# Kernel optimization log

Measured on AMD Instinct MI355X. Metric: run time of the kernel, lower is better.

The kernel has to match this reference:

```python
import jax, jax.numpy as jnp
import numpy as np

D = 512
MOMENTUM = 0.99
NEG_INF = -1.0e9


def setup_inputs() -> dict:
    key = jax.random.key(0)
    ks = jax.random.split(key, 16)
    B, Lq, Lk = 16, 1024, 1024
    s = 0.02
    inp = {
        "uncond_q": jax.random.normal(ks[0], (B, D), jnp.float32),
        "q": jax.random.normal(ks[1], (B, Lq, D), jnp.float32),
        "k": jax.random.normal(ks[2], (B, Lk, D), jnp.float32),
        "v": jax.random.normal(ks[3], (B, Lk, D), jnp.float32),
        "src_key_padding_mask": jax.random.randint(ks[4], (B, Lk), 0, 2) > 0,
        "fallback_score": jnp.zeros((1,), jnp.float32),
        # parameters (torch Linear: y = x @ W.T + b)
        "Wv": jax.random.normal(ks[5], (D, D), jnp.float32) * s,
        "bv": jnp.zeros((D,), jnp.float32),
        "Wf": jax.random.normal(ks[6], (D, D), jnp.float32) * s,
        "bf": jnp.zeros((D,), jnp.float32),
        "W1": jax.random.normal(ks[7], (D, D), jnp.float32) * s,
        "b1": jnp.zeros((D,), jnp.float32),
        "W2": jax.random.normal(ks[8], (D // 2, D), jnp.float32) * s,
        "b2": jnp.zeros((D // 2,), jnp.float32),
        "W3": jax.random.normal(ks[9], (1, D // 2), jnp.float32) * s,
        "b3": jnp.zeros((1,), jnp.float32),
    }
    return inp


def _scorer(x, W1, b1, W2, b2, W3, b3):
    h = jax.nn.relu(x @ W1.T + b1)
    h = jax.nn.relu(h @ W2.T + b2)
    return jnp.tanh(h @ W3.T + b3)


def reference(uncond_q, q, k, v, src_key_padding_mask, fallback_score,
              Wv, bv, Wf, bf, W1, b1, W2, b2, W3, b3):
    B, Lq, _ = q.shape
    v_p = v @ Wv.T + bv                                  # [B,Lk,D]
    default_values = (uncond_q @ Wf.T + bf)[:, None, :]  # [B,1,D]

    scores = jnp.einsum('bqd,bkd->bqk', q, k) / jnp.sqrt(jnp.float32(D))

    # EMA fallback-score update (training mode), detached from grads
    bmax = jax.lax.stop_gradient(scores.max())
    bmin = jax.lax.stop_gradient(scores.min())
    fb = MOMENTUM * fallback_score[0] + (1.0 - MOMENTUM) * (bmax + bmin) / 2.0

    scores = jnp.where(src_key_padding_mask[:, None, :], NEG_INF, scores)
    fb_col = jnp.broadcast_to(fb, (B, Lq, 1))
    scores = jnp.concatenate([scores, fb_col], axis=-1)   # [B,Lq,Lk+1]
    weights = jax.nn.softmax(scores, axis=-1)

    v_padded = jnp.concatenate([v_p, default_values], axis=1)  # [B,Lk+1,D]
    out = jnp.einsum('bqk,bkd->bqd', weights, v_padded)

    return (_scorer(out, W1, b1, W2, b2, W3, b3),
            _scorer(default_values, W1, b1, W2, b2, W3, b3))
```

## Files before the change

### kernel.cpp

```cpp
#include <hip/hip_runtime.h>

typedef _Float16 f16;
typedef f16  f16x8 __attribute__((ext_vector_type(8)));
typedef f16  f16x4 __attribute__((ext_vector_type(4)));
typedef float f32x4 __attribute__((ext_vector_type(4)));

__device__ __forceinline__ void gld_lds16(const f16* g, void* l) {
  __builtin_amdgcn_global_load_lds((const __attribute__((address_space(1))) void*)g,
                                   (__attribute__((address_space(3))) void*)l,
                                   16, 0, 0);
}

enum { EPI_SCORES = 0, EPI_RELU = 2, EPI_OUT = 3, EPI_BIASR = 4 };

template<int EPI, bool XMAP>
__global__ __launch_bounds__(256)
void gemm_bt(const f16* __restrict__ A, const f16* __restrict__ B, void* __restrict__ C,
             int lda, int ldb, int ldc, int K,
             long long sA, long long sB, long long sC,
             const float* __restrict__ bias, float scale,
             float* __restrict__ mmarr, int nmm,
             const float* __restrict__ wfb, const float* __restrict__ dvv,
             int nx, int nbz)
{
  __shared__ __align__(16) f16 As[3][128][32];
  __shared__ __align__(16) f16 Bs[3][128][32];
  const int tid  = threadIdx.x;
  const int lane = tid & 63;
  const int w    = tid >> 6;
  const int wm   = w >> 1, wn = w & 1;

  const int lin = blockIdx.x;
  int bz, bj;
  if constexpr (XMAP) {
    const int xcd = lin & 7, rest = lin >> 3;
    const int grp = rest / nbz;
    bj = rest - grp * nbz;
    bz = xcd + (grp << 3);
  } else {
    bz = lin / nbz; bj = lin - bz * nbz;
  }
  const int m0 = (bj / nx) * 128, n0 = (bj % nx) * 128;
  const f16* Ab = A + (size_t)bz * sA + (size_t)m0 * lda;
  const f16* Bb = B + (size_t)bz * sB + (size_t)n0 * ldb;

  f32x4 acc[4][4] = {};
  const int nsteps = K >> 5;

#define STAGE(bufb, ks)                                                              \
  {                                                                                  \
    const int k0_ = (ks) << 5;                                                       \
    _Pragma("unroll")                                                                \
    for (int i = 0; i < 2; ++i) {                                                    \
      const int ci = i * 256 + tid;                                                  \
      const int r  = ci >> 2;                                                        \
      const int sg = (ci & 3) ^ ((r >> 1) & 3);                                      \
      gld_lds16(Ab + (size_t)r * lda + k0_ + sg * 8,                                 \
                (char*)As + (bufb) + (size_t)(i * 256 + w * 64) * 16);               \
      gld_lds16(Bb + (size_t)r * ldb + k0_ + sg * 8,                                 \
                (char*)Bs + (bufb) + (size_t)(i * 256 + w * 64) * 16);               \
    }                                                                                \
  }

  STAGE(0, 0)
  STAGE(8192, 1)

  const int elemoff = (((lane >> 4) ^ ((lane >> 1) & 3)) << 3);

  int cur = 0;
  for (int t = 0; t < nsteps; ++t) {
    if (t + 1 < nsteps) asm volatile("s_waitcnt vmcnt(4)" ::: "memory");
    else                asm volatile("s_waitcnt vmcnt(0)" ::: "memory");
    __builtin_amdgcn_s_barrier();
    __builtin_amdgcn_sched_barrier(0);
    int st = cur + 2; if (st >= 3) st -= 3;
    if (t + 2 < nsteps) STAGE(st * 8192, t + 2)
    f16x8 af[4], bfr[4];
#pragma unroll
    for (int m = 0; m < 4; ++m)
      af[m] = *(const f16x8*)&As[cur][wm * 64 + m * 16 + (lane & 15)][elemoff];
#pragma unroll
    for (int n = 0; n < 4; ++n)
      bfr[n] = *(const f16x8*)&Bs[cur][wn * 64 + n * 16 + (lane & 15)][elemoff];
    __builtin_amdgcn_s_setprio(1);
#pragma unroll
    for (int m = 0; m < 4; ++m)
#pragma unroll
      for (int n = 0; n < 4; ++n)
        acc[m][n] = __builtin_amdgcn_mfma_f32_16x16x32_f16(af[m], bfr[n], acc[m][n], 0, 0, 0);
    __builtin_amdgcn_s_setprio(0);
    cur = (cur + 1 == 3) ? 0 : cur + 1;
  }
#undef STAGE

  const int col_l = lane & 15;
  const int row_l = (lane >> 4) << 2;

  {
    f16* Ch = (f16*)C + (size_t)bz * sC + (size_t)m0 * ldc + n0;
#pragma unroll
    for (int m = 0; m < 4; ++m)
#pragma unroll
      for (int n = 0; n < 4; ++n)
#pragma unroll
        for (int r = 0; r < 4; ++r) {
          const int rr = wm * 64 + m * 16 + row_l + r;
          const int cc = wn * 64 + n * 16 + col_l;
          float val = acc[m][n][r];
          if constexpr (EPI == EPI_RELU) { val += bias[n0 + cc]; val = fmaxf(val, 0.0f); }
          if constexpr (EPI == EPI_BIASR) val += bias[m0 + rr];
          if constexpr (EPI == EPI_OUT)
            val += wfb[bz * 1024 + m0 + rr] * dvv[bz * 512 + n0 + cc];
          Ch[(size_t)rr * ldc + cc] = (f16)val;
        }
  }
  (void)scale; (void)mmarr; (void)nmm;
}

__global__ __launch_bounds__(512, 2)
void gemm256_scores(const f16* __restrict__ A, const f16* __restrict__ B, f16* __restrict__ C,
                    float scale, float* __restrict__ mmarr)
{
  __shared__ __align__(16) f16 As[3][256][32];
  __shared__ __align__(16) f16 Bs[3][256][32];
  __shared__ float redm[8], redn[8];
  const int tid  = threadIdx.x;
  const int lane = tid & 63;
  const int w    = tid >> 6;
  const int wm   = w >> 2, wn = w & 3;
  const int lin  = blockIdx.x;
  const int xcd = lin & 7, rest = lin >> 3;
  const int bj  = rest & 15;
  const int bz  = xcd + ((rest >> 4) << 3);
  const int m0 = (bj >> 2) * 256, n0 = (bj & 3) * 256;
  const f16* Ab = A + (size_t)bz * 524288 + (size_t)m0 * 512;
  const f16* Bb = B + (size_t)bz * 524288 + (size_t)n0 * 512;

  f32x4 acc[8][4] = {};

#define STAGE2(bufb, ks)                                                             \
  {                                                                                  \
    const int k0_ = (ks) << 5;                                                       \
    _Pragma("unroll")                                                                \
    for (int i = 0; i < 2; ++i) {                                                    \
      const int ci = i * 512 + tid;                                                  \
      const int r  = ci >> 2;                                                        \
      const int sg = (ci & 3) ^ ((r >> 1) & 3);                                      \
      gld_lds16(Ab + (size_t)r * 512 + k0_ + sg * 8,                                 \
                (char*)As + (bufb) + (size_t)(i * 512 + w * 64) * 16);               \
      gld_lds16(Bb + (size_t)r * 512 + k0_ + sg * 8,                                 \
                (char*)Bs + (bufb) + (size_t)(i * 512 + w * 64) * 16);               \
    }                                                                                \
  }

  STAGE2(0, 0)
  STAGE2(16384, 1)

  const int elemoff = (((lane >> 4) ^ ((lane >> 1) & 3)) << 3);

  int cur = 0;
  for (int t = 0; t < 16; ++t) {
    if (t + 1 < 16) asm volatile("s_waitcnt vmcnt(4)" ::: "memory");
    else            asm volatile("s_waitcnt vmcnt(0)" ::: "memory");
    __builtin_amdgcn_s_barrier();
    __builtin_amdgcn_sched_barrier(0);
    int st = cur + 2; if (st >= 3) st -= 3;
    if (t + 2 < 16) STAGE2(st * 16384, t + 2)
    f16x8 af[8], bfr[4];
#pragma unroll
    for (int m = 0; m < 8; ++m)
      af[m] = *(const f16x8*)&As[cur][wm * 128 + m * 16 + (lane & 15)][elemoff];
#pragma unroll
    for (int n = 0; n < 4; ++n)
      bfr[n] = *(const f16x8*)&Bs[cur][wn * 64 + n * 16 + (lane & 15)][elemoff];
    __builtin_amdgcn_s_setprio(1);
#pragma unroll
    for (int m = 0; m < 8; ++m)
#pragma unroll
      for (int n = 0; n < 4; ++n)
        acc[m][n] = __builtin_amdgcn_mfma_f32_16x16x32_f16(af[m], bfr[n], acc[m][n], 0, 0, 0);
    __builtin_amdgcn_s_setprio(0);
    cur = (cur + 1 == 3) ? 0 : cur + 1;
  }
#undef STAGE2

  const int col_l = lane & 15;
  const int row_l = (lane >> 4) << 2;
  f16* Ch = C + (size_t)bz * 1048576 + (size_t)m0 * 1024 + n0;
  float lmax = -3.402823466e38f, lmin = 3.402823466e38f;
#pragma unroll
  for (int m = 0; m < 8; ++m)
#pragma unroll
    for (int n = 0; n < 4; ++n)
#pragma unroll
      for (int r = 0; r < 4; ++r) {
        float val = acc[m][n][r] * scale;
        lmax = fmaxf(lmax, val); lmin = fminf(lmin, val);
        Ch[(size_t)(wm * 128 + m * 16 + row_l + r) * 1024 + (wn * 64 + n * 16 + col_l)] = (f16)val;
      }
#pragma unroll
  for (int off = 32; off >= 1; off >>= 1) {
    lmax = fmaxf(lmax, __shfl_xor(lmax, off));
    lmin = fminf(lmin, __shfl_xor(lmin, off));
  }
  if (lane == 0) { redm[w] = lmax; redn[w] = lmin; }
  __syncthreads();
  if (tid == 0) {
    float gm = redm[0], gn = redn[0];
#pragma unroll
    for (int i = 1; i < 8; ++i) { gm = fmaxf(gm, redm[i]); gn = fminf(gn, redn[i]); }
    mmarr[lin] = gm; mmarr[256 + lin] = gn;
  }
}

__global__ __launch_bounds__(256)
void reduce_mm(const float* __restrict__ mmarr, int n,
               const float* __restrict__ fallback, float* __restrict__ fbv,
               const unsigned char* __restrict__ mask, unsigned* __restrict__ mm)
{
  __shared__ float rm[4], rn[4];
  __shared__ int redc[256];
  const int lane = threadIdx.x & 63, w = threadIdx.x >> 6;
  float mx = -3.402823466e38f, mn = 3.402823466e38f;
  for (int i = threadIdx.x; i < n; i += 256) {
    mx = fmaxf(mx, mmarr[i]);
    mn = fminf(mn, mmarr[n + i]);
  }
#pragma unroll
  for (int off = 32; off >= 1; off >>= 1) {
    mx = fmaxf(mx, __shfl_xor(mx, off));
    mn = fminf(mn, __shfl_xor(mn, off));
  }
  if (lane == 0) { rm[w] = mx; rn[w] = mn; }
  int c = 0;
  for (int i = threadIdx.x; i < 16384; i += 256) c += (mask[i] != 0) ? 1 : 0;
  redc[threadIdx.x] = c;
  __syncthreads();
  for (int s = 128; s > 0; s >>= 1) {
    if (threadIdx.x < s) redc[threadIdx.x] += redc[threadIdx.x + s];
    __syncthreads();
  }
  if (threadIdx.x == 0) {
    float gmax = fmaxf(fmaxf(rm[0], rm[1]), fmaxf(rm[2], rm[3]));
    float gmin = fminf(fminf(rn[0], rn[1]), fminf(rn[2], rn[3]));
    fbv[0] = 0.99f * fallback[0] + 0.005f * (gmax + gmin);
    mm[0] = (unsigned)redc[0];
  }
}

__global__ __launch_bounds__(256)
void conv3_k(const float* __restrict__ a, const float* __restrict__ b,
             const float* __restrict__ c,
             f16* __restrict__ oa, f16* __restrict__ ob, f16* __restrict__ oc)
{
  const int blk = blockIdx.x;
  const int s   = blk >> 10;
  const int lb  = blk & 1023;
  const float* src = (s == 0) ? a : ((s == 1) ? b : c);
  f16*         dst = (s == 0) ? oa : ((s == 1) ? ob : oc);
  const size_t base = (size_t)lb * 8192 + threadIdx.x * 8;
  float4 v0a = *(const float4*)(src + base);
  float4 v0b = *(const float4*)(src + base + 4);
  float4 v1a = *(const float4*)(src + base + 2048);
  float4 v1b = *(const float4*)(src + base + 2052);
  float4 v2a = *(const float4*)(src + base + 4096);
  float4 v2b = *(const float4*)(src + base + 4100);
  float4 v3a = *(const float4*)(src + base + 6144);
  float4 v3b = *(const float4*)(src + base + 6148);
  f16x8 o0 = { (f16)v0a.x,(f16)v0a.y,(f16)v0a.z,(f16)v0a.w,(f16)v0b.x,(f16)v0b.y,(f16)v0b.z,(f16)v0b.w };
  *(f16x8*)(dst + base) = o0;
  f16x8 o1 = { (f16)v1a.x,(f16)v1a.y,(f16)v1a.z,(f16)v1a.w,(f16)v1b.x,(f16)v1b.y,(f16)v1b.z,(f16)v1b.w };
  *(f16x8*)(dst + base + 2048) = o1;
  f16x8 o2 = { (f16)v2a.x,(f16)v2a.y,(f16)v2a.z,(f16)v2a.w,(f16)v2b.x,(f16)v2b.y,(f16)v2b.z,(f16)v2b.w };
  *(f16x8*)(dst + base + 4096) = o2;
  f16x8 o3 = { (f16)v3a.x,(f16)v3a.y,(f16)v3a.z,(f16)v3a.w,(f16)v3b.x,(f16)v3b.y,(f16)v3b.z,(f16)v3b.w };
  *(f16x8*)(dst + base + 6144) = o3;
}

__global__ __launch_bounds__(256)
void convw_k(const float* __restrict__ wv, const float* __restrict__ w1,
             const float* __restrict__ w2,
             f16* __restrict__ owv, f16* __restrict__ ow1, f16* __restrict__ ow2)
{
  int i = blockIdx.x * 256 + threadIdx.x;
  const float* src; f16* dst; int j;
  if (i < 65536)       { src = wv; dst = owv; j = i; }
  else if (i < 131072) { src = w1; dst = ow1; j = i - 65536; }
  else                 { src = w2; dst = ow2; j = i - 131072; }
  float4 v = *(const float4*)(src + (size_t)j * 4);
  f16x4 o = { (f16)v.x, (f16)v.y, (f16)v.z, (f16)v.w };
  *(f16x4*)(dst + (size_t)j * 4) = o;
}

__global__ __launch_bounds__(256)
void softmax_rows(const f16* __restrict__ scores, const void* __restrict__ maskp,
                  const float* __restrict__ fbv, const unsigned* __restrict__ mm,
                  f16* __restrict__ Wt, float* __restrict__ wfb)
{
  __shared__ float red[8];
  const int row  = blockIdx.x;
  const int b    = row >> 10;
  const int tid  = threadIdx.x;
  const int lane = tid & 63, w = tid >> 6;
  const float fb = fbv[0];
  const unsigned mode = (mm[0] > 5000u) ? 1u : 0u;
  const f16* s = scores + (size_t)row * 1024;
  const int k0 = tid * 4;
  f16x4 sv = *(const f16x4*)(s + k0);
  float x[4];
  if (mode) {
    const unsigned char* m8 = (const unsigned char*)maskp + b * 1024 + k0;
    x[0] = m8[0] ? -1e9f : (float)sv[0];  x[1] = m8[1] ? -1e9f : (float)sv[1];
    x[2] = m8[2] ? -1e9f : (float)sv[2];  x[3] = m8[3] ? -1e9f : (float)sv[3];
  } else {
    const int* mi = (const int*)maskp + b * 1024 + k0;
    x[0] = mi[0] ? -1e9f : (float)sv[0];  x[1] = mi[1] ? -1e9f : (float)sv[1];
    x[2] = mi[2] ? -1e9f : (float)sv[2];  x[3] = mi[3] ? -1e9f : (float)sv[3];
  }
  float mx = fmaxf(fmaxf(x[0], x[1]), fmaxf(x[2], x[3]));
#pragma unroll
  for (int off = 32; off >= 1; off >>= 1) mx = fmaxf(mx, __shfl_xor(mx, off));
  if (lane == 0) red[w] = mx;
  __syncthreads();
  mx = fmaxf(fmaxf(fmaxf(red[0], red[1]), fmaxf(red[2], red[3])), fb);
  float e0 = expf(x[0] - mx), e1 = expf(x[1] - mx), e2 = expf(x[2] - mx), e3 = expf(x[3] - mx);
  float sum = (e0 + e1) + (e2 + e3);
#pragma unroll
  for (int off = 32; off >= 1; off >>= 1) sum += __shfl_xor(sum, off);
  if (lane == 0) red[4 + w] = sum;
  __syncthreads();
  float efb = expf(fb - mx);
  float Z = ((red[4] + red[5]) + (red[6] + red[7])) + efb;
  float inv = 1.0f / Z;
  f16x4 o = { (f16)(e0 * inv), (f16)(e1 * inv), (f16)(e2 * inv), (f16)(e3 * inv) };
  *(f16x4*)&Wt[(size_t)row * 1024 + k0] = o;
  if (tid == 0) wfb[row] = efb * inv;
}

template<int IN, int ACT>
__global__ __launch_bounds__(256)
void fc_wave(const float* __restrict__ X, const float* __restrict__ W,
             const float* __restrict__ bias, float* __restrict__ Y, int OutN)
{
  const int gw   = (blockIdx.x * 256 + threadIdx.x) >> 6;
  const int lane = threadIdx.x & 63;
  const int b = gw / OutN, j = gw - b * OutN;
  const float* x  = X + (size_t)b * IN;
  const float* wr = W + (size_t)j * IN;
  float s = 0.f;
  if constexpr (IN == 512) {
    const int o = lane * 8;
    float4 x0 = *(const float4*)(x + o),  x1 = *(const float4*)(x + o + 4);
    float4 w0 = *(const float4*)(wr + o), w1 = *(const float4*)(wr + o + 4);
    s = x0.x*w0.x + x0.y*w0.y + x0.z*w0.z + x0.w*w0.w
      + x1.x*w1.x + x1.y*w1.y + x1.z*w1.z + x1.w*w1.w;
  } else {
    const int o = lane * 4;
    float4 x0 = *(const float4*)(x + o);
    float4 w0 = *(const float4*)(wr + o);
    s = x0.x*w0.x + x0.y*w0.y + x0.z*w0.z + x0.w*w0.w;
  }
#pragma unroll
  for (int off = 32; off >= 1; off >>= 1) s += __shfl_xor(s, off);
  if (lane == 0) {
    float val = s + bias[ACT == 2 ? 0 : j];
    if constexpr (ACT == 1) val = fmaxf(val, 0.f);
    if constexpr (ACT == 2) val = tanhf(val);
    Y[gw] = val;
  }
}

__global__ __launch_bounds__(256)
void y_kernel(const f16* __restrict__ h2, const float* __restrict__ W3,
              const float* __restrict__ b3, float* __restrict__ outp)
{
  int row = blockIdx.x * 16 + (threadIdx.x >> 4);
  int l   = threadIdx.x & 15;
  const f16* h = h2 + (size_t)row * 256 + l * 16;
  float s = 0.f;
#pragma unroll
  for (int j = 0; j < 16; ++j) s += (float)h[j] * W3[l * 16 + j];
#pragma unroll
  for (int off = 1; off < 16; off <<= 1) s += __shfl_xor(s, off);
  if (l == 0) outp[row] = tanhf(s + b3[0]);
}

extern "C" void kernel_launch(void* const* d_in, const int* in_sizes, int n_in,
                              void* d_out, int out_size, void* d_ws, size_t ws_size,
                              hipStream_t stream) {
  const float* uq       = (const float*)d_in[0];
  const float* q        = (const float*)d_in[1];
  const float* kk       = (const float*)d_in[2];
  const float* v        = (const float*)d_in[3];
  const void*  mask     = d_in[4];
  const float* fallback = (const float*)d_in[5];
  const float* Wv = (const float*)d_in[6];
  const float* bv = (const float*)d_in[7];
  const float* Wf = (const float*)d_in[8];
  const float* bf = (const float*)d_in[9];
  const float* W1 = (const float*)d_in[10];
  const float* b1 = (const float*)d_in[11];
  const float* W2 = (const float*)d_in[12];
  const float* b2 = (const float*)d_in[13];
  const float* W3 = (const float*)d_in[14];
  const float* b3 = (const float*)d_in[15];
  float* outp = (float*)d_out;

  char* ws = (char*)d_ws;
  const size_t MB = 1ull << 20;
  f16*  scores = (f16*)ws;
  f16*  h1b  = (f16*)ws;
  f16*  h2b  = (f16*)(ws + 16 * MB);
  f16*  vpt  = (f16*)(ws + 32 * MB);
  f16*  outb = (f16*)(ws + 48 * MB);
  f16*  q16  = (f16*)(ws + 64 * MB);
  f16*  wts  = (f16*)(ws + 64 * MB);
  f16*  k16  = (f16*)(ws + 80 * MB);
  f16*  v16  = (f16*)(ws + 96 * MB);
  char* cst  = ws + 112 * MB;
  f16*  Wv16 = (f16*)(cst);
  f16*  W116 = (f16*)(cst + 512 * 1024);
  f16*  W216 = (f16*)(cst + 1024 * 1024);
  float* dv   = (float*)(cst + 1280 * 1024);
  float* wfb  = (float*)(cst + 1312 * 1024);
  float* h1d  = (float*)(cst + 1376 * 1024);
  float* h2d  = (float*)(cst + 1408 * 1024);
  unsigned* mm = (unsigned*)(cst + 1424 * 1024);
  float* fbv   = (float*)(cst + 1428 * 1024);
  float* mmarr = (float*)(cst + 1432 * 1024);

  conv3_k<<<3072, 256, 0, stream>>>(q, kk, v, q16, k16, v16);
  convw_k<<<640, 256, 0, stream>>>(Wv, W1, W2, Wv16, W116, W216);

  fc_wave<512, 0><<<2048, 256, 0, stream>>>(uq, Wf, bf, dv, 512);

  gemm256_scores<<<256, 512, 0, stream>>>(q16, k16, scores, 0.04419417382415922f, mmarr);

  reduce_mm<<<1, 256, 0, stream>>>(mmarr, 256, fallback, fbv,
                                   (const unsigned char*)mask, mm);

  softmax_rows<<<16384, 256, 0, stream>>>(scores, mask, fbv, mm, wts, wfb);

  gemm_bt<EPI_BIASR, true><<<512, 256, 0, stream>>>(
      Wv16, v16, vpt, 512, 512, 1024, 512,
      0LL, 524288LL, 524288LL,
      bv, 1.f, nullptr, 0, nullptr, nullptr, 8, 32);

  gemm_bt<EPI_OUT, true><<<512, 256, 0, stream>>>(
      wts, vpt, outb, 1024, 1024, 512, 1024,
      1048576LL, 524288LL, 524288LL,
      nullptr, 1.f, nullptr, 0, wfb, dv, 4, 32);

  gemm_bt<EPI_RELU, false><<<512, 256, 0, stream>>>(
      outb, W116, h1b, 512, 512, 512, 512, 0LL, 0LL, 0LL,
      b1, 1.f, nullptr, 0, nullptr, nullptr, 4, 512);

  gemm_bt<EPI_RELU, false><<<256, 256, 0, stream>>>(
      h1b, W216, h2b, 512, 512, 256, 512, 0LL, 0LL, 0LL,
      b2, 1.f, nullptr, 0, nullptr, nullptr, 2, 256);

  y_kernel<<<1024, 256, 0, stream>>>(h2b, W3, b3, outp);

  fc_wave<512, 1><<<2048, 256, 0, stream>>>(dv, W1, b1, h1d, 512);
  fc_wave<512, 1><<<1024, 256, 0, stream>>>(h1d, W2, b2, h2d, 256);
  fc_wave<256, 2><<<4, 256, 0, stream>>>(h2d, W3, b3, outp + 16384, 1);

  (void)in_sizes; (void)n_in; (void)out_size; (void)ws_size;
}
```

Before: 180.7 us.

## Fuse fp32-to-fp16 conversion of q and k into the scores GEMM

The scores GEMM now loads fp32 q and k straight into LDS through global_load_lds and converts them to fp16 in registers when fragments are read, so the separate conversion pass over q and k is dropped. The standalone conversion kernel now handles only v. To fit the fp32 tiles in LDS the pipeline goes from three stages to two, with an extra barrier before each refill. The GEMM moves twice as many bytes per tile and has less prefetch depth, which may expose memory latency, but it avoids writing and re-reading fp16 copies of q and k.

After: 175.1 us. -3.1%, faster.

```diff
diff --git a/kernel.cpp b/kernel.cpp
--- a/kernel.cpp
+++ b/kernel.cpp
@@ -3,12 +3,27 @@
 typedef _Float16 f16;
 typedef f16  f16x8 __attribute__((ext_vector_type(8)));
 typedef f16  f16x4 __attribute__((ext_vector_type(4)));
+typedef __fp16 fp16x2 __attribute__((ext_vector_type(2)));
 typedef float f32x4 __attribute__((ext_vector_type(4)));
 
 __device__ __forceinline__ void gld_lds16(const f16* g, void* l) {
   __builtin_amdgcn_global_load_lds((const __attribute__((address_space(1))) void*)g,
                                    (__attribute__((address_space(3))) void*)l,
                                    16, 0, 0);
+}
+__device__ __forceinline__ void gld_lds16f(const float* g, void* l) {
+  __builtin_amdgcn_global_load_lds((const __attribute__((address_space(1))) void*)g,
+                                   (__attribute__((address_space(3))) void*)l,
+                                   16, 0, 0);
+}
+
+__device__ __forceinline__ f16x8 pack8(float4 a, float4 b) {
+  union { f16x8 v; fp16x2 h[4]; } u;
+  u.h[0] = __builtin_amdgcn_cvt_pkrtz(a.x, a.y);
+  u.h[1] = __builtin_amdgcn_cvt_pkrtz(a.z, a.w);
+  u.h[2] = __builtin_amdgcn_cvt_pkrtz(b.x, b.y);
+  u.h[3] = __builtin_amdgcn_cvt_pkrtz(b.z, b.w);
+  return u.v;
 }
 
 enum { EPI_SCORES = 0, EPI_RELU = 2, EPI_OUT = 3, EPI_BIASR = 4 };
@@ -118,11 +133,11 @@
 }
 
 __global__ __launch_bounds__(512, 2)
-void gemm256_scores(const f16* __restrict__ A, const f16* __restrict__ B, f16* __restrict__ C,
+void gemm256_scores(const float* __restrict__ A, const float* __restrict__ B, f16* __restrict__ C,
                     float scale, float* __restrict__ mmarr)
 {
-  __shared__ __align__(16) f16 As[3][256][32];
-  __shared__ __align__(16) f16 Bs[3][256][32];
+  __shared__ __align__(16) float AsF[2][256][32];
+  __shared__ __align__(16) float BsF[2][256][32];
   __shared__ float redm[8], redn[8];
   const int tid  = threadIdx.x;
   const int lane = tid & 63;
@@ -133,46 +148,51 @@
   const int bj  = rest & 15;
   const int bz  = xcd + ((rest >> 4) << 3);
   const int m0 = (bj >> 2) * 256, n0 = (bj & 3) * 256;
-  const f16* Ab = A + (size_t)bz * 524288 + (size_t)m0 * 512;
-  const f16* Bb = B + (size_t)bz * 524288 + (size_t)n0 * 512;
+  const float* Ab = A + (size_t)bz * 524288 + (size_t)m0 * 512;
+  const float* Bb = B + (size_t)bz * 524288 + (size_t)n0 * 512;
 
   f32x4 acc[8][4] = {};
 
-#define STAGE2(bufb, ks)                                                             \
+#define STAGEF(bufb, ks)                                                             \
   {                                                                                  \
     const int k0_ = (ks) << 5;                                                       \
     _Pragma("unroll")                                                                \
-    for (int i = 0; i < 2; ++i) {                                                    \
+    for (int i = 0; i < 4; ++i) {                                                    \
       const int ci = i * 512 + tid;                                                  \
-      const int r  = ci >> 2;                                                        \
-      const int sg = (ci & 3) ^ ((r >> 1) & 3);                                      \
-      gld_lds16(Ab + (size_t)r * 512 + k0_ + sg * 8,                                 \
-                (char*)As + (bufb) + (size_t)(i * 512 + w * 64) * 16);               \
-      gld_lds16(Bb + (size_t)r * 512 + k0_ + sg * 8,                                 \
-                (char*)Bs + (bufb) + (size_t)(i * 512 + w * 64) * 16);               \
+      const int r  = ci >> 3;                                                        \
+      const int sg = (ci & 7) ^ (((ci >> 4) & 3) << 1);                              \
+      gld_lds16f(Ab + (size_t)r * 512 + k0_ + sg * 4,                                \
+                 (char*)AsF + (bufb) + (size_t)ci * 16);                             \
+      gld_lds16f(Bb + (size_t)r * 512 + k0_ + sg * 4,                                \
+                 (char*)BsF + (bufb) + (size_t)ci * 16);                             \
     }                                                                                \
   }
 
-  STAGE2(0, 0)
-  STAGE2(16384, 1)
-
-  const int elemoff = (((lane >> 4) ^ ((lane >> 1) & 3)) << 3);
+  STAGEF(0, 0)
+  STAGEF(32768, 1)
+
+  const int fr = lane & 15;
+  const int eo = (((lane >> 4) ^ ((lane >> 1) & 3)) << 3);
 
   int cur = 0;
   for (int t = 0; t < 16; ++t) {
-    if (t + 1 < 16) asm volatile("s_waitcnt vmcnt(4)" ::: "memory");
-    else            asm volatile("s_waitcnt vmcnt(0)" ::: "memory");
+    if (t < 15) asm volatile("s_waitcnt vmcnt(8)" ::: "memory");
+    else        asm volatile("s_waitcnt vmcnt(0)" ::: "memory");
     __builtin_amdgcn_s_barrier();
     __builtin_amdgcn_sched_barrier(0);
-    int st = cur + 2; if (st >= 3) st -= 3;
-    if (t + 2 < 16) STAGE2(st * 16384, t + 2)
+    const float* Ac = (const float*)((const char*)AsF + cur * 32768);
+    const float* Bc = (const float*)((const char*)BsF + cur * 32768);
     f16x8 af[8], bfr[4];
 #pragma unroll
-    for (int m = 0; m < 8; ++m)
-      af[m] = *(const f16x8*)&As[cur][wm * 128 + m * 16 + (lane & 15)][elemoff];
-#pragma unroll
-    for (int n = 0; n < 4; ++n)
-      bfr[n] = *(const f16x8*)&Bs[cur][wn * 64 + n * 16 + (lane & 15)][elemoff];
+    for (int m = 0; m < 8; ++m) {
+      const float* p = Ac + (size_t)(wm * 128 + m * 16 + fr) * 32 + eo;
+      af[m] = pack8(*(const float4*)p, *(const float4*)(p + 4));
+    }
+#pragma unroll
+    for (int n = 0; n < 4; ++n) {
+      const float* p = Bc + (size_t)(wn * 64 + n * 16 + fr) * 32 + eo;
+      bfr[n] = pack8(*(const float4*)p, *(const float4*)(p + 4));
+    }
     __builtin_amdgcn_s_setprio(1);
 #pragma unroll
     for (int m = 0; m < 8; ++m)
@@ -180,9 +200,11 @@
       for (int n = 0; n < 4; ++n)
         acc[m][n] = __builtin_amdgcn_mfma_f32_16x16x32_f16(af[m], bfr[n], acc[m][n], 0, 0, 0);
     __builtin_amdgcn_s_setprio(0);
-    cur = (cur + 1 == 3) ? 0 : cur + 1;
-  }
-#undef STAGE2
+    __builtin_amdgcn_s_barrier();
+    if (t + 2 < 16) STAGEF(cur * 32768, t + 2)
+    cur ^= 1;
+  }
+#undef STAGEF
 
   const int col_l = lane & 15;
   const int row_l = (lane >> 4) << 2;
@@ -249,32 +271,16 @@
 }
 
 __global__ __launch_bounds__(256)
-void conv3_k(const float* __restrict__ a, const float* __restrict__ b,
-             const float* __restrict__ c,
-             f16* __restrict__ oa, f16* __restrict__ ob, f16* __restrict__ oc)
-{
-  const int blk = blockIdx.x;
-  const int s   = blk >> 10;
-  const int lb  = blk & 1023;
-  const float* src = (s == 0) ? a : ((s == 1) ? b : c);
-  f16*         dst = (s == 0) ? oa : ((s == 1) ? ob : oc);
-  const size_t base = (size_t)lb * 8192 + threadIdx.x * 8;
-  float4 v0a = *(const float4*)(src + base);
-  float4 v0b = *(const float4*)(src + base + 4);
-  float4 v1a = *(const float4*)(src + base + 2048);
-  float4 v1b = *(const float4*)(src + base + 2052);
-  float4 v2a = *(const float4*)(src + base + 4096);
-  float4 v2b = *(const float4*)(src + base + 4100);
-  float4 v3a = *(const float4*)(src + base + 6144);
-  float4 v3b = *(const float4*)(src + base + 6148);
-  f16x8 o0 = { (f16)v0a.x,(f16)v0a.y,(f16)v0a.z,(f16)v0a.w,(f16)v0b.x,(f16)v0b.y,(f16)v0b.z,(f16)v0b.w };
-  *(f16x8*)(dst + base) = o0;
-  f16x8 o1 = { (f16)v1a.x,(f16)v1a.y,(f16)v1a.z,(f16)v1a.w,(f16)v1b.x,(f16)v1b.y,(f16)v1b.z,(f16)v1b.w };
-  *(f16x8*)(dst + base + 2048) = o1;
-  f16x8 o2 = { (f16)v2a.x,(f16)v2a.y,(f16)v2a.z,(f16)v2a.w,(f16)v2b.x,(f16)v2b.y,(f16)v2b.z,(f16)v2b.w };
-  *(f16x8*)(dst + base + 4096) = o2;
-  f16x8 o3 = { (f16)v3a.x,(f16)v3a.y,(f16)v3a.z,(f16)v3a.w,(f16)v3b.x,(f16)v3b.y,(f16)v3b.z,(f16)v3b.w };
-  *(f16x8*)(dst + base + 6144) = o3;
+void conv_v(const float* __restrict__ v, f16* __restrict__ v16)
+{
+  const int i = blockIdx.x * 256 + threadIdx.x;
+#pragma unroll
+  for (int it = 0; it < 4; ++it) {
+    const size_t j = (size_t)i + (size_t)it * 524288;
+    float4 x = *(const float4*)(v + j * 4);
+    f16x4 o = { (f16)x.x, (f16)x.y, (f16)x.z, (f16)x.w };
+    *(f16x4*)(v16 + j * 4) = o;
+  }
 }
 
 __global__ __launch_bounds__(256)
@@ -413,9 +419,7 @@
   f16*  h2b  = (f16*)(ws + 16 * MB);
   f16*  vpt  = (f16*)(ws + 32 * MB);
   f16*  outb = (f16*)(ws + 48 * MB);
-  f16*  q16  = (f16*)(ws + 64 * MB);
   f16*  wts  = (f16*)(ws + 64 * MB);
-  f16*  k16  = (f16*)(ws + 80 * MB);
   f16*  v16  = (f16*)(ws + 96 * MB);
   char* cst  = ws + 112 * MB;
   f16*  Wv16 = (f16*)(cst);
@@ -429,12 +433,12 @@
   float* fbv   = (float*)(cst + 1428 * 1024);
   float* mmarr = (float*)(cst + 1432 * 1024);
 
-  conv3_k<<<3072, 256, 0, stream>>>(q, kk, v, q16, k16, v16);
+  conv_v<<<2048, 256, 0, stream>>>(v, v16);
   convw_k<<<640, 256, 0, stream>>>(Wv, W1, W2, Wv16, W116, W216);
 
   fc_wave<512, 0><<<2048, 256, 0, stream>>>(uq, Wf, bf, dv, 512);
 
-  gemm256_scores<<<256, 512, 0, stream>>>(q16, k16, scores, 0.04419417382415922f, mmarr);
+  gemm256_scores<<<256, 512, 0, stream>>>(q, kk, scores, 0.04419417382415922f, mmarr);
 
   reduce_mm<<<1, 256, 0, stream>>>(mmarr, 256, fallback, fbv,
                                    (const unsigned char*)mask, mm);
```
